# Kernel optimization log

Measured on AMD Instinct MI355X. Metric: run time of the kernel, lower is better.

Reference implementation:

```python
import jax, jax.numpy as jnp
import numpy as np

N_HEAD = 16

def setup_inputs() -> dict:
    key = jax.random.key(0)
    k1, k2, k3 = jax.random.split(key, 3)
    B, T, C = 4, 2048, 1024
    x = jax.random.normal(k1, (B, T, C), dtype=jnp.float32)
    w_attn = jax.random.normal(k2, (C, 3 * C), dtype=jnp.float32) * 0.02
    w_o = jax.random.normal(k3, (C, C), dtype=jnp.float32) * 0.02
    return {"x": x, "w_attn": w_attn, "w_o": w_o}

def reference(x, w_attn, w_o):
    B, T, C = x.shape
    H = N_HEAD
    hs = C // H
    qkv = x @ w_attn  # [B,T,3C]
    q, k, v = jnp.split(qkv, 3, axis=-1)
    # [B,H,T,hs]
    q = q.reshape(B, T, H, hs).transpose(0, 2, 1, 3)
    k = k.reshape(B, T, H, hs).transpose(0, 2, 1, 3)
    v = v.reshape(B, T, H, hs).transpose(0, 2, 1, 3)
    att = jnp.einsum('bhqd,bhkd->bhqk', q, k) * (1.0 / np.sqrt(hs).astype(np.float32))
    causal = jnp.tril(jnp.ones((T, T), dtype=bool))
    att = jnp.where(causal[None, None], att, jnp.float32(-jnp.inf))
    att = jax.nn.softmax(att, axis=-1)
    y = jnp.einsum('bhqk,bhkd->bhqd', att, v)
    y = y.transpose(0, 2, 1, 3).reshape(B, T, C)
    return y @ w_o
```

## Files before the change

### kernel.cpp

```cpp
#include <hip/hip_runtime.h>

typedef unsigned short u16;
typedef unsigned int u32;
typedef __attribute__((ext_vector_type(8))) __bf16 bf16x8;
typedef __attribute__((ext_vector_type(4))) float f32x4;
typedef __attribute__((ext_vector_type(8))) unsigned short u16x8;
typedef __attribute__((ext_vector_type(4))) unsigned int u32x4;

typedef const __attribute__((address_space(1))) u32 gu32;
typedef __attribute__((address_space(3))) u32 lu32;

__device__ __forceinline__ u16 f2b(float f) {
  u32 u = __builtin_bit_cast(u32, f);
  u32 r = u + 0x7fffu + ((u >> 16) & 1u);
  return (u16)(r >> 16);
}

__device__ __forceinline__ u32 pk2(float lo, float hi) {
  u32 d;
  asm("v_cvt_pk_bf16_f32 %0, %1, %2" : "=v"(d) : "v"(lo), "v"(hi));
  return d;
}

__device__ __forceinline__ bf16x8 pack8(f32x4 a, f32x4 b) {
  u32x4 u;
  u[0] = pk2(a[0], a[1]);
  u[1] = pk2(a[2], a[3]);
  u[2] = pk2(b[0], b[1]);
  u[3] = pk2(b[2], b[3]);
  return __builtin_bit_cast(bf16x8, u);
}

__device__ __forceinline__ bf16x8 ld8(const u16* p) {
  return __builtin_bit_cast(bf16x8, *(const u16x8*)p);
}

__device__ __forceinline__ void gll16(const void* g, void* l) {
  __builtin_amdgcn_global_load_lds((gu32*)g, (lu32*)l, 16, 0, 0);
}

__device__ __forceinline__ f32x4 mfma16(bf16x8 a, bf16x8 b, f32x4 c) {
  return __builtin_amdgcn_mfma_f32_16x16x32_bf16(a, b, c, 0, 0, 0);
}

__global__ void k_cvt(const float* __restrict__ in, u16* __restrict__ out, int n4) {
  int i = blockIdx.x * blockDim.x + threadIdx.x;
  int stride = gridDim.x * blockDim.x;
  for (int idx = i; idx < n4; idx += stride) {
    float4 v = ((const float4*)in)[idx];
    u32 lo = (u32)f2b(v.x) | ((u32)f2b(v.y) << 16);
    u32 hi = (u32)f2b(v.z) | ((u32)f2b(v.w) << 16);
    ((uint2*)out)[idx] = make_uint2(lo, hi);
  }
}

__global__ void k_tr2(const float* __restrict__ in0, u16* __restrict__ out0,
                      const float* __restrict__ in1, u16* __restrict__ out1) {
  __shared__ u16 tile[32][33];
  int bxr = blockIdx.x;
  const float* in;
  u16* out;
  int C, bx;
  if (bxr < 96) {
    in = in0; out = out0; C = 3072; bx = bxr * 32;
  } else {
    in = in1; out = out1; C = 1024; bx = (bxr - 96) * 32;
  }
  const int R = 1024;
  int by = blockIdx.y * 32;
  int tx = threadIdx.x, ty = threadIdx.y;
#pragma unroll
  for (int i = 0; i < 32; i += 8)
    tile[ty + i][tx] = f2b(in[(size_t)(by + ty + i) * C + bx + tx]);
  __syncthreads();
#pragma unroll
  for (int i = 0; i < 32; i += 8)
    out[(size_t)(bx + ty + i) * R + by + tx] = tile[tx][ty + i];
}

template <int EPI>
__global__ __launch_bounds__(256) void k_gemm(const u16* __restrict__ A,
                                              const u16* __restrict__ B,
                                              void* __restrict__ Cp) {
  const int K = 1024;
  const int NT = 32;
  __shared__ __align__(16) u16 As[2][128 * 32];
  __shared__ __align__(16) u16 Bs[2][128 * 32];
  int tid = threadIdx.x;
  int lane = tid & 63, wid = tid >> 6;
  int wr = wid >> 1, wc = wid & 1;

  int nwgx = gridDim.x;
  int bid = blockIdx.y * nwgx + blockIdx.x;
  int cpx = (nwgx * gridDim.y) >> 3;
  int sb = (bid & 7) * cpx + (bid >> 3);
  int m0 = (sb / nwgx) * 128, n0 = (sb % nwgx) * 128;

  int r = lane & 15, qq = lane >> 4;

  int schunk = (lane & 3) ^ ((lane >> 3) & 3);
  const u16* Ag0 = A + (size_t)(m0 + wid * 32 + (lane >> 2)) * K + schunk * 8;
  const u16* Bg0 = B + (size_t)(n0 + wid * 32 + (lane >> 2)) * K + schunk * 8;
  int sl0 = (wid * 32) * 32;
  int sl1 = (wid * 32 + 16) * 32;
  int rsw = (qq ^ ((r >> 1) & 3)) * 8;

#define GSTAGE(buf, k0)                          \
  do {                                           \
    gll16(Ag0 + (k0), &As[buf][sl0]);            \
    gll16(Ag0 + 16 * K + (k0), &As[buf][sl1]);   \
    gll16(Bg0 + (k0), &Bs[buf][sl0]);            \
    gll16(Bg0 + 16 * K + (k0), &Bs[buf][sl1]);   \
  } while (0)

  f32x4 acc[4][4] = {};

  GSTAGE(0, 0);
  GSTAGE(1, 32);

  for (int kt = 0; kt < NT; ++kt) {
    int cur = kt & 1;
    if (kt + 1 < NT)
      asm volatile("s_waitcnt vmcnt(4)" ::: "memory");
    else
      asm volatile("s_waitcnt vmcnt(0)" ::: "memory");
    __builtin_amdgcn_s_barrier();

    bf16x8 af[4], bfr[4];
#pragma unroll
    for (int m = 0; m < 4; ++m)
      af[m] = ld8(&As[cur][(wr * 64 + m * 16 + r) * 32 + rsw]);
#pragma unroll
    for (int n = 0; n < 4; ++n)
      bfr[n] = ld8(&Bs[cur][(wc * 64 + n * 16 + r) * 32 + rsw]);
    asm volatile("s_waitcnt lgkmcnt(0)" ::: "memory");
    __builtin_amdgcn_sched_barrier(0);
    __builtin_amdgcn_s_barrier();

    if (kt + 2 < NT) GSTAGE(cur, (kt + 2) * 32);

#pragma unroll
    for (int m = 0; m < 4; ++m)
#pragma unroll
      for (int n = 0; n < 4; ++n) acc[m][n] = mfma16(af[m], bfr[n], acc[m][n]);
  }
#undef GSTAGE

  if constexpr (EPI == 0) {
    u16* qkv = (u16*)Cp;
#pragma unroll
    for (int m = 0; m < 4; ++m) {
      int gr = m0 + wr * 64 + m * 16 + qq * 4;
      int b = gr >> 11, t0 = gr & 2047;
#pragma unroll
      for (int n = 0; n < 4; ++n) {
        int gc = n0 + wc * 64 + n * 16 + r;
        int which = gc >> 10, rem = gc & 1023;
        int hh = rem >> 6, d = rem & 63;
        if (which == 2) {
          u16* dst = qkv + (size_t)2 * 8388608u +
                     ((size_t)((b * 16 + hh) * 64 + d)) * 2048 + t0;
          u32 p0 = pk2(acc[m][n][0], acc[m][n][1]);
          u32 p1 = pk2(acc[m][n][2], acc[m][n][3]);
          *(uint2*)dst = make_uint2(p0, p1);
        } else {
          float sc = (which == 0) ? 0.18033688011112042f : 1.0f;
          u16* dst = qkv + (size_t)which * 8388608u +
                     ((size_t)((b * 16 + hh) * 2048 + t0)) * 64 + d;
#pragma unroll
          for (int i = 0; i < 4; ++i) dst[(size_t)i * 64] = f2b(acc[m][n][i] * sc);
        }
      }
    }
  } else {
    float* out = (float*)Cp;
#pragma unroll
    for (int m = 0; m < 4; ++m) {
      int gr = m0 + wr * 64 + m * 16 + qq * 4;
#pragma unroll
      for (int n = 0; n < 4; ++n) {
        int gc = n0 + wc * 64 + n * 16 + r;
#pragma unroll
        for (int i = 0; i < 4; ++i) out[(size_t)(gr + i) * 1024 + gc] = acc[m][n][i];
      }
    }
  }
}

__global__ __launch_bounds__(512) void k_attn(const u16* __restrict__ Qm,
                                              const u16* __restrict__ Km,
                                              const u16* __restrict__ VTm,
                                              u16* __restrict__ Y) {
  int bi = blockIdx.x;
  int p = bi >> 6;
  int bh = bi & 63;
  int b = bh >> 4, h = bh & 15;
  int tid = threadIdx.x, lane = tid & 63, w = tid >> 6;
  int g = w >> 2, wl = w & 3;
  int r = lane & 15, qq = lane >> 4;
  const size_t base = (size_t)bh * (2048 * 64);

  __shared__ __align__(16) u16 Kt[2][2][64 * 64];
  __shared__ __align__(16) u16 Vt[2][2][64 * 64];

  int srow = lane >> 3;
  int kch0 = (lane & 7) ^ (srow & 3);
  int kch1 = (lane & 7) ^ ((srow & 3) | 4);
  int vch = (lane & 7) ^ srow;
  const u16* Kg = Km + base;
  const u16* Vg = VTm + base;

  int ar = 8 * (r >> 2) + (r & 3);
  int fkl = (r & 3) | (((r >> 2) & 1) << 2);
  int ks0 = ((qq ^ fkl)) * 8, ks1 = ((qq ^ fkl) ^ 4) * 8;
  int fvl = r & 7;
  int vs0 = ((qq ^ fvl)) * 8, vs1 = ((qq ^ fvl) ^ 4) * 8;

#define STAGE(par, j0n)                                                                 \
  do {                                                                                  \
    gll16(Kg + (size_t)((j0n) + wl * 16 + srow) * 64 + kch0 * 8,                        \
          &Kt[par][g][(wl * 16) * 64]);                                                 \
    gll16(Kg + (size_t)((j0n) + wl * 16 + 8 + srow) * 64 + kch1 * 8,                    \
          &Kt[par][g][(wl * 16 + 8) * 64]);                                             \
    gll16(Vg + (size_t)(wl * 16 + srow) * 2048 + (j0n) + vch * 8,                       \
          &Vt[par][g][(wl * 16) * 64]);                                                 \
    gll16(Vg + (size_t)(wl * 16 + 8 + srow) * 2048 + (j0n) + vch * 8,                   \
          &Vt[par][g][(wl * 16 + 8) * 64]);                                             \
  } while (0)

  for (int ph = 0; ph < 2; ++ph) {
    int qb = (ph == 0) ? (15 - p) : p;
    int qb0 = qb * 128;
    int q0w = qb0 + wl * 32;

    bf16x8 qf[2][2];
#pragma unroll
    for (int m = 0; m < 2; ++m)
#pragma unroll
      for (int kc = 0; kc < 2; ++kc)
        qf[m][kc] = ld8(Qm + base + (size_t)(q0w + m * 16 + r) * 64 + kc * 32 + qq * 8);

    f32x4 acc[2][4] = {};
    float m_run[2] = {-1e30f, -1e30f};
    float l_run[2] = {0.f, 0.f};
    int npairs = qb + 1;

    STAGE(0, g << 6);
    __syncthreads();

    for (int t2 = 0; t2 < npairs; ++t2) {
      int j0 = (t2 << 7) + (g << 6);
      int cur = t2 & 1;
      bool active = (j0 <= q0w + 31);
      f32x4 s[4][2];
      bf16x8 vfr[4][2];

      if (active) {
        __builtin_amdgcn_s_setprio(1);
#pragma unroll
        for (int nt = 0; nt < 4; ++nt) {
          int knt = 32 * (nt >> 1) + 4 * (nt & 1);
          const u16* kb_ = &Kt[cur][g][(knt + ar) * 64];
          bf16x8 k0 = ld8(kb_ + ks0);
          bf16x8 k1 = ld8(kb_ + ks1);
#pragma unroll
          for (int m = 0; m < 2; ++m) {
            f32x4 z = {};
            s[nt][m] = mfma16(k1, qf[m][1], mfma16(k0, qf[m][0], z));
          }
        }
#pragma unroll
        for (int n = 0; n < 4; ++n) {
          const u16* vb_ = &Vt[cur][g][(n * 16 + r) * 64];
          vfr[n][0] = ld8(vb_ + vs0);
          vfr[n][1] = ld8(vb_ + vs1);
        }
        __builtin_amdgcn_s_setprio(0);
      }

      if (t2 + 1 < npairs) STAGE((t2 + 1) & 1, ((t2 + 1) << 7) + (g << 6));

      if (active) {
        bool nm = (j0 + 63 > q0w);
        if (nm) {
#pragma unroll
          for (int nt = 0; nt < 4; ++nt) {
            int kb = j0 + 32 * (nt >> 1) + 4 * (nt & 1) + 8 * qq;
#pragma unroll
            for (int m = 0; m < 2; ++m) {
              int qg = q0w + m * 16 + r;
#pragma unroll
              for (int i = 0; i < 4; ++i)
                s[nt][m][i] = (kb + i <= qg) ? s[nt][m][i] : -1e30f;
            }
          }
        }

        float tm[2];
#pragma unroll
        for (int m = 0; m < 2; ++m) {
          float t0 = fmaxf(fmaxf(s[0][m][0], s[0][m][1]), fmaxf(s[0][m][2], s[0][m][3]));
          float t1 = fmaxf(fmaxf(s[1][m][0], s[1][m][1]), fmaxf(s[1][m][2], s[1][m][3]));
          float t2f = fmaxf(fmaxf(s[2][m][0], s[2][m][1]), fmaxf(s[2][m][2], s[2][m][3]));
          float t3 = fmaxf(fmaxf(s[3][m][0], s[3][m][1]), fmaxf(s[3][m][2], s[3][m][3]));
          float t = fmaxf(fmaxf(t0, t1), fmaxf(t2f, t3));
          t = fmaxf(t, __shfl_xor(t, 16));
          t = fmaxf(t, __shfl_xor(t, 32));
          tm[m] = t;
        }

        int grow = (tm[0] > m_run[0]) | (tm[1] > m_run[1]);
        if (__any(grow)) {
#pragma unroll
          for (int m = 0; m < 2; ++m) {
            float mn = fmaxf(m_run[m], tm[m]);
            float corr = __builtin_amdgcn_exp2f(m_run[m] - mn);
            m_run[m] = mn;
            l_run[m] *= corr;
#pragma unroll
            for (int i = 0; i < 4; ++i) {
              float c = __shfl(corr, qq * 4 + i);
#pragma unroll
              for (int n = 0; n < 4; ++n) acc[m][n][i] *= c;
            }
          }
        }

#pragma unroll
        for (int m = 0; m < 2; ++m) {
          float ls = 0.f;
#pragma unroll
          for (int nt = 0; nt < 4; ++nt)
#pragma unroll
            for (int i = 0; i < 4; ++i) {
              float e = __builtin_amdgcn_exp2f(s[nt][m][i] - m_run[m]);
              s[nt][m][i] = e;
              ls += e;
            }
          l_run[m] += ls;
        }

        __builtin_amdgcn_s_setprio(1);
#pragma unroll
        for (int m = 0; m < 2; ++m) {
          bf16x8 pa0 = pack8(s[0][m], s[1][m]);
          bf16x8 pa1 = pack8(s[2][m], s[3][m]);
#pragma unroll
          for (int n = 0; n < 4; ++n) acc[m][n] = mfma16(pa0, vfr[n][0], acc[m][n]);
#pragma unroll
          for (int n = 0; n < 4; ++n) acc[m][n] = mfma16(pa1, vfr[n][1], acc[m][n]);
        }
        __builtin_amdgcn_s_setprio(0);
      }

      __syncthreads();
    }

    float lfin[2];
#pragma unroll
    for (int m = 0; m < 2; ++m) {
      float l = l_run[m];
      l += __shfl_xor(l, 16);
      l += __shfl_xor(l, 32);
      lfin[m] = l;
    }

    float* mgK = (float*)&Kt[0][0][0];
    float* mgV = (float*)&Vt[0][0][0];
    int offA = wl * 1104 + lane * 17;
    int offM = 4608 + wl * 320 + lane * 5;
    if (g == 1) {
#pragma unroll
      for (int n = 0; n < 4; ++n)
#pragma unroll
        for (int i = 0; i < 4; ++i) {
          mgK[offA + n * 4 + i] = acc[0][n][i];
          mgV[offA + n * 4 + i] = acc[1][n][i];
        }
      mgK[offM + 0] = m_run[0];
      mgK[offM + 1] = m_run[1];
      mgK[offM + 2] = lfin[0];
      mgK[offM + 3] = lfin[1];
    }
    __syncthreads();

    if (g == 0) {
      float fA[2], fB[2];
#pragma unroll
      for (int m = 0; m < 2; ++m) {
        float mB = mgK[offM + m];
        float lB = mgK[offM + 2 + m];
        float mM = fmaxf(m_run[m], mB);
        float cA = __builtin_amdgcn_exp2f(m_run[m] - mM);
        float cB = __builtin_amdgcn_exp2f(mB - mM);
        float inv = 1.0f / (lfin[m] * cA + lB * cB);
        fA[m] = cA * inv;
        fB[m] = cB * inv;
      }
#pragma unroll
      for (int m = 0; m < 2; ++m)
#pragma unroll
        for (int i = 0; i < 4; ++i) {
          float a = __shfl(fA[m], qq * 4 + i);
          float bq = __shfl(fB[m], qq * 4 + i);
          float* mg = (m == 0) ? mgK : mgV;
#pragma unroll
          for (int n = 0; n < 4; ++n) {
            float o = acc[m][n][i] * a + mg[offA + n * 4 + i] * bq;
            Y[((size_t)(b * 2048 + q0w + m * 16 + qq * 4 + i)) * 1024 + h * 64 +
              n * 16 + r] = f2b(o);
          }
        }
    }
    __syncthreads();
  }
#undef STAGE
}

extern "C" void kernel_launch(void* const* d_in, const int* in_sizes, int n_in,
                              void* d_out, int out_size, void* d_ws, size_t ws_size,
                              hipStream_t stream) {
  const float* x = (const float*)d_in[0];
  const float* w_attn = (const float*)d_in[1];
  const float* w_o = (const float*)d_in[2];
  float* out = (float*)d_out;

  char* ws = (char*)d_ws;
  u16* xb = (u16*)(ws + 0);
  u16* watT = (u16*)(ws + 16777216);
  u16* woT = (u16*)(ws + 23068672);
  u16* qb = (u16*)(ws + 25165824);
  u16* kb = (u16*)(ws + 41943040);
  u16* vb = (u16*)(ws + 58720256);
  u16* yb = (u16*)(ws + 75497472);

  k_cvt<<<2048, 256, 0, stream>>>(x, xb, 8192 * 1024 / 4);
  k_tr2<<<dim3(128, 32), dim3(32, 8), 0, stream>>>(w_attn, watT, w_o, woT);
  k_gemm<0><<<dim3(24, 64), 256, 0, stream>>>(xb, watT, (void*)qb);
  k_attn<<<dim3(512), 512, 0, stream>>>(qb, kb, vb, yb);
  k_gemm<1><<<dim3(8, 64), 256, 0, stream>>>(yb, woT, (void*)out);
}
```

Measured before the change: 177.7 us.

## Fuse fp32-to-bf16 conversion of x into the QKV GEMM A-tile loads

Removes the separate conversion kernel for x. The QKV GEMM now loads fp32 A tiles into registers, packs them to bf16 and writes them to LDS. B tiles keep using async global_load_lds. This saves a kernel launch and a full write and read of the bf16 copy of x. In exchange the GEMM reads twice as many A bytes on every tile re-read and loses the asynchronous LDS load path for A. Waiting on vmcnt inside the loop before the MFMAs may expose load latency.

```diff
diff --git a/kernel.cpp b/kernel.cpp
--- a/kernel.cpp
+++ b/kernel.cpp
@@ -41,17 +41,6 @@
 
 __device__ __forceinline__ f32x4 mfma16(bf16x8 a, bf16x8 b, f32x4 c) {
   return __builtin_amdgcn_mfma_f32_16x16x32_bf16(a, b, c, 0, 0, 0);
-}
-
-__global__ void k_cvt(const float* __restrict__ in, u16* __restrict__ out, int n4) {
-  int i = blockIdx.x * blockDim.x + threadIdx.x;
-  int stride = gridDim.x * blockDim.x;
-  for (int idx = i; idx < n4; idx += stride) {
-    float4 v = ((const float4*)in)[idx];
-    u32 lo = (u32)f2b(v.x) | ((u32)f2b(v.y) << 16);
-    u32 hi = (u32)f2b(v.z) | ((u32)f2b(v.w) << 16);
-    ((uint2*)out)[idx] = make_uint2(lo, hi);
-  }
 }
 
 __global__ void k_tr2(const float* __restrict__ in0, u16* __restrict__ out0,
@@ -79,7 +68,7 @@
 }
 
 template <int EPI>
-__global__ __launch_bounds__(256) void k_gemm(const u16* __restrict__ A,
+__global__ __launch_bounds__(256) void k_gemm(const void* __restrict__ Ap,
                                               const u16* __restrict__ B,
                                               void* __restrict__ Cp) {
   const int K = 1024;
@@ -99,52 +88,128 @@
   int r = lane & 15, qq = lane >> 4;
 
   int schunk = (lane & 3) ^ ((lane >> 3) & 3);
-  const u16* Ag0 = A + (size_t)(m0 + wid * 32 + (lane >> 2)) * K + schunk * 8;
-  const u16* Bg0 = B + (size_t)(n0 + wid * 32 + (lane >> 2)) * K + schunk * 8;
+  int arow = wid * 32 + (lane >> 2);
+  const u16* Bg0 = B + (size_t)(n0 + arow) * K + schunk * 8;
   int sl0 = (wid * 32) * 32;
-  int sl1 = (wid * 32 + 16) * 32;
+  int sl1 = sl0 + 16 * 32;
   int rsw = (qq ^ ((r >> 1) & 3)) * 8;
+  int awo = sl0 + (lane >> 2) * 32 + (lane & 3) * 8;
+
+  f32x4 acc[4][4] = {};
+
+#define BG(buf, k0)                              \
+  do {                                           \
+    gll16(Bg0 + (k0), &Bs[buf][sl0]);            \
+    gll16(Bg0 + 16 * K + (k0), &Bs[buf][sl1]);   \
+  } while (0)
+
+  if constexpr (EPI == 0) {
+    const float* Af = (const float*)Ap;
+    const float* Agf0 = Af + (size_t)(m0 + arow) * K + schunk * 8;
+    const float* Agf1 = Agf0 + (size_t)16 * K;
+    float4 av0, av1, av2, av3;
+
+#define AISSUE(k0)                               \
+  do {                                           \
+    av0 = *(const float4*)(Agf0 + (k0));         \
+    av1 = *(const float4*)(Agf0 + (k0) + 4);     \
+    av2 = *(const float4*)(Agf1 + (k0));         \
+    av3 = *(const float4*)(Agf1 + (k0) + 4);     \
+  } while (0)
+#define AWRITE(buf)                                            \
+  do {                                                         \
+    u32x4 w0, w1;                                              \
+    w0[0] = pk2(av0.x, av0.y); w0[1] = pk2(av0.z, av0.w);      \
+    w0[2] = pk2(av1.x, av1.y); w0[3] = pk2(av1.z, av1.w);      \
+    w1[0] = pk2(av2.x, av2.y); w1[1] = pk2(av2.z, av2.w);      \
+    w1[2] = pk2(av3.x, av3.y); w1[3] = pk2(av3.z, av3.w);      \
+    *(u32x4*)&As[buf][awo] = w0;                               \
+    *(u32x4*)&As[buf][awo + 16 * 32] = w1;                     \
+  } while (0)
+
+    AISSUE(0);
+    BG(0, 0);
+    asm volatile("s_waitcnt vmcnt(2)" ::: "memory");
+    AWRITE(0);
+    AISSUE(32);
+    BG(1, 32);
+    asm volatile("s_waitcnt vmcnt(2)" ::: "memory");
+    AWRITE(1);
+
+    for (int kt = 0; kt < NT; ++kt) {
+      int cur = kt & 1;
+      if (kt + 2 < NT) AISSUE((kt + 2) * 32);
+      if (kt == NT - 1) asm volatile("s_waitcnt vmcnt(0)" ::: "memory");
+      asm volatile("s_waitcnt lgkmcnt(0)" ::: "memory");
+      __builtin_amdgcn_s_barrier();
+
+      bf16x8 af[4], bfr[4];
+#pragma unroll
+      for (int m = 0; m < 4; ++m)
+        af[m] = ld8(&As[cur][(wr * 64 + m * 16 + r) * 32 + rsw]);
+#pragma unroll
+      for (int n = 0; n < 4; ++n)
+        bfr[n] = ld8(&Bs[cur][(wc * 64 + n * 16 + r) * 32 + rsw]);
+      asm volatile("s_waitcnt lgkmcnt(0)" ::: "memory");
+      __builtin_amdgcn_sched_barrier(0);
+      __builtin_amdgcn_s_barrier();
+
+      if (kt + 2 < NT) {
+        BG(cur, (kt + 2) * 32);
+        asm volatile("s_waitcnt vmcnt(2)" ::: "memory");
+        AWRITE(cur);
+      }
+
+#pragma unroll
+      for (int m = 0; m < 4; ++m)
+#pragma unroll
+        for (int n = 0; n < 4; ++n) acc[m][n] = mfma16(af[m], bfr[n], acc[m][n]);
+    }
+#undef AISSUE
+#undef AWRITE
+  } else {
+    const u16* Ab = (const u16*)Ap;
+    const u16* Ag0 = Ab + (size_t)(m0 + arow) * K + schunk * 8;
 
 #define GSTAGE(buf, k0)                          \
   do {                                           \
     gll16(Ag0 + (k0), &As[buf][sl0]);            \
     gll16(Ag0 + 16 * K + (k0), &As[buf][sl1]);   \
-    gll16(Bg0 + (k0), &Bs[buf][sl0]);            \
-    gll16(Bg0 + 16 * K + (k0), &Bs[buf][sl1]);   \
+    BG(buf, k0);                                 \
   } while (0)
 
-  f32x4 acc[4][4] = {};
-
-  GSTAGE(0, 0);
-  GSTAGE(1, 32);
-
-  for (int kt = 0; kt < NT; ++kt) {
-    int cur = kt & 1;
-    if (kt + 1 < NT)
-      asm volatile("s_waitcnt vmcnt(4)" ::: "memory");
-    else
-      asm volatile("s_waitcnt vmcnt(0)" ::: "memory");
-    __builtin_amdgcn_s_barrier();
-
-    bf16x8 af[4], bfr[4];
-#pragma unroll
-    for (int m = 0; m < 4; ++m)
-      af[m] = ld8(&As[cur][(wr * 64 + m * 16 + r) * 32 + rsw]);
-#pragma unroll
-    for (int n = 0; n < 4; ++n)
-      bfr[n] = ld8(&Bs[cur][(wc * 64 + n * 16 + r) * 32 + rsw]);
-    asm volatile("s_waitcnt lgkmcnt(0)" ::: "memory");
-    __builtin_amdgcn_sched_barrier(0);
-    __builtin_amdgcn_s_barrier();
-
-    if (kt + 2 < NT) GSTAGE(cur, (kt + 2) * 32);
-
-#pragma unroll
-    for (int m = 0; m < 4; ++m)
-#pragma unroll
-      for (int n = 0; n < 4; ++n) acc[m][n] = mfma16(af[m], bfr[n], acc[m][n]);
+    GSTAGE(0, 0);
+    GSTAGE(1, 32);
+
+    for (int kt = 0; kt < NT; ++kt) {
+      int cur = kt & 1;
+      if (kt + 1 < NT)
+        asm volatile("s_waitcnt vmcnt(4)" ::: "memory");
+      else
+        asm volatile("s_waitcnt vmcnt(0)" ::: "memory");
+      __builtin_amdgcn_s_barrier();
+
+      bf16x8 af[4], bfr[4];
+#pragma unroll
+      for (int m = 0; m < 4; ++m)
+        af[m] = ld8(&As[cur][(wr * 64 + m * 16 + r) * 32 + rsw]);
+#pragma unroll
+      for (int n = 0; n < 4; ++n)
+        bfr[n] = ld8(&Bs[cur][(wc * 64 + n * 16 + r) * 32 + rsw]);
+      asm volatile("s_waitcnt lgkmcnt(0)" ::: "memory");
+      __builtin_amdgcn_sched_barrier(0);
+      __builtin_amdgcn_s_barrier();
+
+      if (kt + 2 < NT) GSTAGE(cur, (kt + 2) * 32);
+
+#pragma unroll
+      for (int m = 0; m < 4; ++m)
+#pragma unroll
+        for (int n = 0; n < 4; ++n) acc[m][n] = mfma16(af[m], bfr[n], acc[m][n]);
+    }
+#undef GSTAGE
   }
-#undef GSTAGE
+#undef BG
 
   if constexpr (EPI == 0) {
     u16* qkv = (u16*)Cp;
@@ -426,7 +491,6 @@
   float* out = (float*)d_out;
 
   char* ws = (char*)d_ws;
-  u16* xb = (u16*)(ws + 0);
   u16* watT = (u16*)(ws + 16777216);
   u16* woT = (u16*)(ws + 23068672);
   u16* qb = (u16*)(ws + 25165824);
@@ -434,9 +498,8 @@
   u16* vb = (u16*)(ws + 58720256);
   u16* yb = (u16*)(ws + 75497472);
 
-  k_cvt<<<2048, 256, 0, stream>>>(x, xb, 8192 * 1024 / 4);
   k_tr2<<<dim3(128, 32), dim3(32, 8), 0, stream>>>(w_attn, watT, w_o, woT);
-  k_gemm<0><<<dim3(24, 64), 256, 0, stream>>>(xb, watT, (void*)qb);
+  k_gemm<0><<<dim3(24, 64), 256, 0, stream>>>((const void*)x, watT, (void*)qb);
   k_attn<<<dim3(512), 512, 0, stream>>>(qb, kb, vb, yb);
-  k_gemm<1><<<dim3(8, 64), 256, 0, stream>>>(yb, woT, (void*)out);
-}
+  k_gemm<1><<<dim3(8, 64), 256, 0, stream>>>((const void*)yb, woT, (void*)out);
+}
```

Measured after the change: 178.8 us. About the same (+0.6%).

## Fuse fp32-to-bf16 conversion of x into QKV GEMM A-operand loading

Applied to the files above, without the earlier changes.

Removes the standalone x conversion kernel and has the QKV GEMM read fp32 x directly. Loads go to registers three stages ahead, and the kernel converts them with v_cvt_pk_bf16_f32 and writes them to LDS using double-buffered register sets. This drops one kernel launch plus the bf16 write and read-back of x. In exchange the GEMM reads twice as many bytes for A, since each tile is re-read in fp32 by 24 column blocks. It also takes more registers and more complex vmcnt accounting.

```diff
diff --git a/kernel.cpp b/kernel.cpp
--- a/kernel.cpp
+++ b/kernel.cpp
@@ -41,17 +41,6 @@
 
 __device__ __forceinline__ f32x4 mfma16(bf16x8 a, bf16x8 b, f32x4 c) {
   return __builtin_amdgcn_mfma_f32_16x16x32_bf16(a, b, c, 0, 0, 0);
-}
-
-__global__ void k_cvt(const float* __restrict__ in, u16* __restrict__ out, int n4) {
-  int i = blockIdx.x * blockDim.x + threadIdx.x;
-  int stride = gridDim.x * blockDim.x;
-  for (int idx = i; idx < n4; idx += stride) {
-    float4 v = ((const float4*)in)[idx];
-    u32 lo = (u32)f2b(v.x) | ((u32)f2b(v.y) << 16);
-    u32 hi = (u32)f2b(v.z) | ((u32)f2b(v.w) << 16);
-    ((uint2*)out)[idx] = make_uint2(lo, hi);
-  }
 }
 
 __global__ void k_tr2(const float* __restrict__ in0, u16* __restrict__ out0,
@@ -79,7 +68,7 @@
 }
 
 template <int EPI>
-__global__ __launch_bounds__(256) void k_gemm(const u16* __restrict__ A,
+__global__ __launch_bounds__(256) void k_gemm(const void* __restrict__ Ap,
                                               const u16* __restrict__ B,
                                               void* __restrict__ Cp) {
   const int K = 1024;
@@ -99,52 +88,154 @@
   int r = lane & 15, qq = lane >> 4;
 
   int schunk = (lane & 3) ^ ((lane >> 3) & 3);
-  const u16* Ag0 = A + (size_t)(m0 + wid * 32 + (lane >> 2)) * K + schunk * 8;
-  const u16* Bg0 = B + (size_t)(n0 + wid * 32 + (lane >> 2)) * K + schunk * 8;
+  int arow = wid * 32 + (lane >> 2);
+  const u16* Bg0 = B + (size_t)(n0 + arow) * K + schunk * 8;
   int sl0 = (wid * 32) * 32;
-  int sl1 = (wid * 32 + 16) * 32;
+  int sl1 = sl0 + 16 * 32;
   int rsw = (qq ^ ((r >> 1) & 3)) * 8;
+  int awo = sl0 + (lane >> 2) * 32 + (lane & 3) * 8;
+
+  f32x4 acc[4][4] = {};
+
+#define BG(buf, k0)                              \
+  do {                                           \
+    gll16(Bg0 + (k0), &Bs[buf][sl0]);            \
+    gll16(Bg0 + 16 * K + (k0), &Bs[buf][sl1]);   \
+  } while (0)
+
+  if constexpr (EPI == 0) {
+    const float* Af = (const float*)Ap;
+    const float* Agf0 = Af + (size_t)(m0 + arow) * K + schunk * 8;
+    const float* Agf1 = Agf0 + (size_t)16 * K;
+    float4 avA0, avA1, avA2, avA3;
+    float4 avB0, avB1, avB2, avB3;
+
+#define AISSUE_A(k0)                              \
+  do {                                            \
+    avA0 = *(const float4*)(Agf0 + (k0));         \
+    avA1 = *(const float4*)(Agf0 + (k0) + 4);     \
+    avA2 = *(const float4*)(Agf1 + (k0));         \
+    avA3 = *(const float4*)(Agf1 + (k0) + 4);     \
+  } while (0)
+#define AISSUE_B(k0)                              \
+  do {                                            \
+    avB0 = *(const float4*)(Agf0 + (k0));         \
+    avB1 = *(const float4*)(Agf0 + (k0) + 4);     \
+    avB2 = *(const float4*)(Agf1 + (k0));         \
+    avB3 = *(const float4*)(Agf1 + (k0) + 4);     \
+  } while (0)
+#define AWRITE_A(buf)                                              \
+  do {                                                             \
+    u32x4 w0, w1;                                                  \
+    w0[0] = pk2(avA0.x, avA0.y); w0[1] = pk2(avA0.z, avA0.w);      \
+    w0[2] = pk2(avA1.x, avA1.y); w0[3] = pk2(avA1.z, avA1.w);      \
+    w1[0] = pk2(avA2.x, avA2.y); w1[1] = pk2(avA2.z, avA2.w);      \
+    w1[2] = pk2(avA3.x, avA3.y); w1[3] = pk2(avA3.z, avA3.w);      \
+    *(u32x4*)&As[buf][awo] = w0;                                   \
+    *(u32x4*)&As[buf][awo + 16 * 32] = w1;                         \
+  } while (0)
+#define AWRITE_B(buf)                                              \
+  do {                                                             \
+    u32x4 w0, w1;                                                  \
+    w0[0] = pk2(avB0.x, avB0.y); w0[1] = pk2(avB0.z, avB0.w);      \
+    w0[2] = pk2(avB1.x, avB1.y); w0[3] = pk2(avB1.z, avB1.w);      \
+    w1[0] = pk2(avB2.x, avB2.y); w1[1] = pk2(avB2.z, avB2.w);      \
+    w1[2] = pk2(avB3.x, avB3.y); w1[3] = pk2(avB3.z, avB3.w);      \
+    *(u32x4*)&As[buf][awo] = w0;                                   \
+    *(u32x4*)&As[buf][awo + 16 * 32] = w1;                         \
+  } while (0)
+
+#define KBODY(kt, AWR, AIS)                                                   \
+  do {                                                                        \
+    if ((kt) + 3 < NT) AIS(((kt) + 3) * 32);                                  \
+    if ((kt) == NT - 1) asm volatile("s_waitcnt vmcnt(0)" ::: "memory");      \
+    asm volatile("s_waitcnt lgkmcnt(0)" ::: "memory");                        \
+    __builtin_amdgcn_s_barrier();                                             \
+    int cur = (kt) & 1;                                                       \
+    bf16x8 af[4], bfr[4];                                                     \
+    _Pragma("unroll") for (int m = 0; m < 4; ++m)                             \
+        af[m] = ld8(&As[cur][(wr * 64 + m * 16 + r) * 32 + rsw]);             \
+    _Pragma("unroll") for (int n = 0; n < 4; ++n)                             \
+        bfr[n] = ld8(&Bs[cur][(wc * 64 + n * 16 + r) * 32 + rsw]);            \
+    asm volatile("s_waitcnt lgkmcnt(0)" ::: "memory");                        \
+    __builtin_amdgcn_sched_barrier(0);                                        \
+    __builtin_amdgcn_s_barrier();                                             \
+    if ((kt) + 2 < NT) BG(cur, ((kt) + 2) * 32);                              \
+    _Pragma("unroll") for (int m = 0; m < 4; ++m)                             \
+        _Pragma("unroll") for (int n = 0; n < 4; ++n)                         \
+            acc[m][n] = mfma16(af[m], bfr[n], acc[m][n]);                     \
+    __builtin_amdgcn_sched_barrier(0);                                        \
+    if ((kt) + 2 < NT) {                                                      \
+      if ((kt) + 3 < NT)                                                      \
+        asm volatile("s_waitcnt vmcnt(6)" ::: "memory");                      \
+      else                                                                    \
+        asm volatile("s_waitcnt vmcnt(2)" ::: "memory");                      \
+      AWR(cur);                                                               \
+    }                                                                         \
+  } while (0)
+
+    AISSUE_A(0);
+    BG(0, 0);
+    asm volatile("s_waitcnt vmcnt(2)" ::: "memory");
+    AWRITE_A(0);
+    AISSUE_A(32);
+    BG(1, 32);
+    asm volatile("s_waitcnt vmcnt(2)" ::: "memory");
+    AWRITE_A(1);
+    AISSUE_B(64);
+
+    for (int kt = 0; kt < NT; kt += 2) {
+      KBODY(kt, AWRITE_B, AISSUE_A);
+      KBODY(kt + 1, AWRITE_A, AISSUE_B);
+    }
+#undef KBODY
+#undef AISSUE_A
+#undef AISSUE_B
+#undef AWRITE_A
+#undef AWRITE_B
+  } else {
+    const u16* Ab = (const u16*)Ap;
+    const u16* Ag0 = Ab + (size_t)(m0 + arow) * K + schunk * 8;
 
 #define GSTAGE(buf, k0)                          \
   do {                                           \
     gll16(Ag0 + (k0), &As[buf][sl0]);            \
     gll16(Ag0 + 16 * K + (k0), &As[buf][sl1]);   \
-    gll16(Bg0 + (k0), &Bs[buf][sl0]);            \
-    gll16(Bg0 + 16 * K + (k0), &Bs[buf][sl1]);   \
-  } while (0)
-
-  f32x4 acc[4][4] = {};
-
-  GSTAGE(0, 0);
-  GSTAGE(1, 32);
-
-  for (int kt = 0; kt < NT; ++kt) {
-    int cur = kt & 1;
-    if (kt + 1 < NT)
-      asm volatile("s_waitcnt vmcnt(4)" ::: "memory");
-    else
-      asm volatile("s_waitcnt vmcnt(0)" ::: "memory");
-    __builtin_amdgcn_s_barrier();
-
-    bf16x8 af[4], bfr[4];
-#pragma unroll
-    for (int m = 0; m < 4; ++m)
-      af[m] = ld8(&As[cur][(wr * 64 + m * 16 + r) * 32 + rsw]);
-#pragma unroll
-    for (int n = 0; n < 4; ++n)
-      bfr[n] = ld8(&Bs[cur][(wc * 64 + n * 16 + r) * 32 + rsw]);
-    asm volatile("s_waitcnt lgkmcnt(0)" ::: "memory");
-    __builtin_amdgcn_sched_barrier(0);
-    __builtin_amdgcn_s_barrier();
-
-    if (kt + 2 < NT) GSTAGE(cur, (kt + 2) * 32);
-
-#pragma unroll
-    for (int m = 0; m < 4; ++m)
-#pragma unroll
-      for (int n = 0; n < 4; ++n) acc[m][n] = mfma16(af[m], bfr[n], acc[m][n]);
+    BG(buf, k0);                                 \
+  } while (0)
+
+    GSTAGE(0, 0);
+    GSTAGE(1, 32);
+
+    for (int kt = 0; kt < NT; ++kt) {
+      int cur = kt & 1;
+      if (kt + 1 < NT)
+        asm volatile("s_waitcnt vmcnt(4)" ::: "memory");
+      else
+        asm volatile("s_waitcnt vmcnt(0)" ::: "memory");
+      __builtin_amdgcn_s_barrier();
+
+      bf16x8 af[4], bfr[4];
+#pragma unroll
+      for (int m = 0; m < 4; ++m)
+        af[m] = ld8(&As[cur][(wr * 64 + m * 16 + r) * 32 + rsw]);
+#pragma unroll
+      for (int n = 0; n < 4; ++n)
+        bfr[n] = ld8(&Bs[cur][(wc * 64 + n * 16 + r) * 32 + rsw]);
+      asm volatile("s_waitcnt lgkmcnt(0)" ::: "memory");
+      __builtin_amdgcn_sched_barrier(0);
+      __builtin_amdgcn_s_barrier();
+
+      if (kt + 2 < NT) GSTAGE(cur, (kt + 2) * 32);
+
+#pragma unroll
+      for (int m = 0; m < 4; ++m)
+#pragma unroll
+        for (int n = 0; n < 4; ++n) acc[m][n] = mfma16(af[m], bfr[n], acc[m][n]);
+    }
+#undef GSTAGE
   }
-#undef GSTAGE
+#undef BG
 
   if constexpr (EPI == 0) {
     u16* qkv = (u16*)Cp;
@@ -426,7 +517,6 @@
   float* out = (float*)d_out;
 
   char* ws = (char*)d_ws;
-  u16* xb = (u16*)(ws + 0);
   u16* watT = (u16*)(ws + 16777216);
   u16* woT = (u16*)(ws + 23068672);
   u16* qb = (u16*)(ws + 25165824);
@@ -434,9 +524,8 @@
   u16* vb = (u16*)(ws + 58720256);
   u16* yb = (u16*)(ws + 75497472);
 
-  k_cvt<<<2048, 256, 0, stream>>>(x, xb, 8192 * 1024 / 4);
   k_tr2<<<dim3(128, 32), dim3(32, 8), 0, stream>>>(w_attn, watT, w_o, woT);
-  k_gemm<0><<<dim3(24, 64), 256, 0, stream>>>(xb, watT, (void*)qb);
+  k_gemm<0><<<dim3(24, 64), 256, 0, stream>>>((const void*)x, watT, (void*)qb);
   k_attn<<<dim3(512), 512, 0, stream>>>(qb, kb, vb, yb);
-  k_gemm<1><<<dim3(8, 64), 256, 0, stream>>>(yb, woT, (void*)out);
-}
+  k_gemm<1><<<dim3(8, 64), 256, 0, stream>>>((const void*)yb, woT, (void*)out);
+}
```

Measured after the change: 195.7 us. 10.1% more time.
